# Optimization experiments

Hardware: AMD Instinct MI355X
Metric: run time of the kernel (lower is better)

## Reference

```python
import jax, jax.numpy as jnp
import numpy as np

B, MAXF, NFEAT, FT_OUT = 16384, 32, 768, 1024

def setup_inputs() -> dict:
    key = jax.random.key(0)
    k1, k2, k3, k4, k5, k6 = jax.random.split(key, 6)
    values = jnp.ones((B, MAXF), dtype=jnp.float32)
    stm_indices = jax.random.randint(k1, (B, MAXF), 0, NFEAT, dtype=jnp.int32)
    nstm_indices = jax.random.randint(k2, (B, MAXF), 0, NFEAT, dtype=jnp.int32)
    ft_w = jax.random.normal(k3, (NFEAT, FT_OUT), dtype=jnp.float32) * 0.02
    ft_b = jax.random.normal(k4, (FT_OUT,), dtype=jnp.float32) * 0.02
    out_w = jax.random.normal(k5, (2 * FT_OUT, 1), dtype=jnp.float32) * 0.02
    out_b = jax.random.normal(k6, (1,), dtype=jnp.float32) * 0.02
    return {"values": values, "stm_indices": stm_indices, "nstm_indices": nstm_indices,
            "ft_w": ft_w, "ft_b": ft_b, "out_w": out_w, "out_b": out_b}

def _ft_slice(indices, values, ft_w, ft_b):
    # sparse gather-accumulate: [B, MAXF] indices into [NFEAT, FT_OUT] table
    gathered = jnp.take(ft_w, indices, axis=0)          # [B, MAXF, FT_OUT]
    return jnp.einsum('bf,bfd->bd', values, gathered) + ft_b  # [B, FT_OUT]

def reference(values, stm_indices, nstm_indices, ft_w, ft_b, out_w, out_b):
    stm_ft = _ft_slice(stm_indices, values, ft_w, ft_b)
    nstm_ft = _ft_slice(nstm_indices, values, ft_w, ft_b)
    hidden = jnp.clip(jnp.concatenate([stm_ft, nstm_ft], axis=1), 0.0, 1.0)
    return jax.nn.sigmoid(hidden @ out_w + out_b)  # [B, 1]
```

## Files before the change

### kernel.cpp

```cpp
#include <hip/hip_runtime.h>
#include <hip/hip_fp16.h>
#include <math.h>

#define BATCH 16384
#define MAXF 32
#define NFEAT 768
#define FT_OUT 1024
#define CHUNK 32
#define NCHUNK (FT_OUT / CHUNK)
#define GROUPS 24
#define CH_ELEMS (NFEAT * CHUNK)

#define GET4(a, f) (((f) & 3) == 0 ? (a)[(f) >> 2].x : \
                    ((f) & 3) == 1 ? (a)[(f) >> 2].y : \
                    ((f) & 3) == 2 ? (a)[(f) >> 2].z : (a)[(f) >> 2].w)

__global__ __launch_bounds__(256) void convert_kernel(const float* __restrict__ ft_w,
                                                      __half* __restrict__ tab) {
    const int i = (blockIdx.x * 256 + threadIdx.x) * 4;
    const int r = i >> 10;
    const int col = i & 1023;
    const int c = col >> 5;
    const int within = col & 31;
    float4 f = *(const float4*)(ft_w + i);
    __half2 lo = __floats2half2_rn(f.x, f.y);
    __half2 hi = __floats2half2_rn(f.z, f.w);
    __half2* dst = (__half2*)(tab + (size_t)c * CH_ELEMS + r * CHUNK + within);
    dst[0] = lo;
    dst[1] = hi;
}

__global__ __launch_bounds__(256, 3) void nnboard_main(
    const float* __restrict__ values,
    const int*   __restrict__ stm_idx,
    const int*   __restrict__ nstm_idx,
    const __half* __restrict__ tab,
    const float* __restrict__ ft_b,
    const float* __restrict__ out_w,
    float*       __restrict__ logits)
{
    __shared__ __half s_tab[CH_ELEMS];

    const int tid = threadIdx.x;
    const int c = blockIdx.x % NCHUNK;
    const int g = blockIdx.x / NCHUNK;

    {
        const uint4* src = (const uint4*)(tab + (size_t)c * CH_ELEMS);
        uint4* dst = (uint4*)s_tab;
        #pragma unroll
        for (int k = 0; k < CH_ELEMS / 8 / 256; ++k)
            dst[k * 256 + tid] = src[k * 256 + tid];
    }
    __syncthreads();

    const int grp = tid >> 2;
    const int j   = tid & 3;
    const int col0 = c * CHUNK + j * 8;
    const __half* my_tab = s_tab + j * 8;

    const float4 bia0 = *(const float4*)(ft_b + col0);
    const float4 bia1 = *(const float4*)(ft_b + col0 + 4);
    const float4 ws0  = *(const float4*)(out_w + col0);
    const float4 ws1  = *(const float4*)(out_w + col0 + 4);
    const float4 wn0  = *(const float4*)(out_w + FT_OUT + col0);
    const float4 wn1  = *(const float4*)(out_w + FT_OUT + col0 + 4);

    const __half2 zero2 = __float2half2_rn(0.f);

    for (int it = g; it < BATCH / 64; it += GROUPS) {
        const int b = it * 64 + grp;

        const int4*   sp = (const int4*)(stm_idx + b * MAXF);
        const int4*   np = (const int4*)(nstm_idx + b * MAXF);
        const float4* vp = (const float4*)(values + b * MAXF);
        int4 si[8], ni[8];
        float4 vv[8];
        #pragma unroll
        for (int k = 0; k < 8; ++k) { si[k] = sp[k]; ni[k] = np[k]; vv[k] = vp[k]; }

        __half2 accs[4] = {zero2, zero2, zero2, zero2};
        __half2 accn[4] = {zero2, zero2, zero2, zero2};

        #pragma unroll
        for (int f = 0; f < MAXF; ++f) {
            const int is = GET4(si, f);
            const int in = GET4(ni, f);
            const __half2 v2 = __float2half2_rn(GET4(vv, f));
            const uint4 qs = *(const uint4*)(my_tab + is * CHUNK);
            const uint4 qn = *(const uint4*)(my_tab + in * CHUNK);
            accs[0] = __hfma2(*(const __half2*)&qs.x, v2, accs[0]);
            accs[1] = __hfma2(*(const __half2*)&qs.y, v2, accs[1]);
            accs[2] = __hfma2(*(const __half2*)&qs.z, v2, accs[2]);
            accs[3] = __hfma2(*(const __half2*)&qs.w, v2, accs[3]);
            accn[0] = __hfma2(*(const __half2*)&qn.x, v2, accn[0]);
            accn[1] = __hfma2(*(const __half2*)&qn.y, v2, accn[1]);
            accn[2] = __hfma2(*(const __half2*)&qn.z, v2, accn[2]);
            accn[3] = __hfma2(*(const __half2*)&qn.w, v2, accn[3]);
        }

        float p = 0.f;
        {
            const float2 f0 = __half22float2(accs[0]);
            const float2 f1 = __half22float2(accs[1]);
            const float2 f2 = __half22float2(accs[2]);
            const float2 f3 = __half22float2(accs[3]);
            const float2 g0 = __half22float2(accn[0]);
            const float2 g1 = __half22float2(accn[1]);
            const float2 g2 = __half22float2(accn[2]);
            const float2 g3 = __half22float2(accn[3]);
            auto clip = [](float x) { return fminf(fmaxf(x, 0.f), 1.f); };
            p = fmaf(clip(f0.x + bia0.x), ws0.x, p);
            p = fmaf(clip(f0.y + bia0.y), ws0.y, p);
            p = fmaf(clip(f1.x + bia0.z), ws0.z, p);
            p = fmaf(clip(f1.y + bia0.w), ws0.w, p);
            p = fmaf(clip(f2.x + bia1.x), ws1.x, p);
            p = fmaf(clip(f2.y + bia1.y), ws1.y, p);
            p = fmaf(clip(f3.x + bia1.z), ws1.z, p);
            p = fmaf(clip(f3.y + bia1.w), ws1.w, p);
            p = fmaf(clip(g0.x + bia0.x), wn0.x, p);
            p = fmaf(clip(g0.y + bia0.y), wn0.y, p);
            p = fmaf(clip(g1.x + bia0.z), wn0.z, p);
            p = fmaf(clip(g1.y + bia0.w), wn0.w, p);
            p = fmaf(clip(g2.x + bia1.x), wn1.x, p);
            p = fmaf(clip(g2.y + bia1.y), wn1.y, p);
            p = fmaf(clip(g3.x + bia1.z), wn1.z, p);
            p = fmaf(clip(g3.y + bia1.w), wn1.w, p);
        }

        p += __shfl_down(p, 1, 64);
        p += __shfl_down(p, 2, 64);
        if (j == 0) atomicAdd(logits + b, p);
    }
}

__global__ __launch_bounds__(256) void sigmoid_kernel(const float* __restrict__ logits,
                                                      const float* __restrict__ out_b,
                                                      float* __restrict__ out) {
    const int i = blockIdx.x * 256 + threadIdx.x;
    out[i] = 1.f / (1.f + expf(-(logits[i] + out_b[0])));
}

extern "C" void kernel_launch(void* const* d_in, const int* in_sizes, int n_in,
                              void* d_out, int out_size, void* d_ws, size_t ws_size,
                              hipStream_t stream) {
    const float* values   = (const float*)d_in[0];
    const int*   stm_idx  = (const int*)d_in[1];
    const int*   nstm_idx = (const int*)d_in[2];
    const float* ft_w     = (const float*)d_in[3];
    const float* ft_b     = (const float*)d_in[4];
    const float* out_w    = (const float*)d_in[5];
    const float* out_b    = (const float*)d_in[6];
    float*       out      = (float*)d_out;

    __half* tab    = (__half*)d_ws;
    float*  logits = (float*)((char*)d_ws + (size_t)NCHUNK * CH_ELEMS * 2);

    convert_kernel<<<(NFEAT * FT_OUT) / (256 * 4), 256, 0, stream>>>(ft_w, tab);
    hipMemsetAsync(logits, 0, BATCH * sizeof(float), stream);
    nnboard_main<<<NCHUNK * GROUPS, 256, 0, stream>>>(
        values, stm_idx, nstm_idx, tab, ft_b, out_w, logits);
    sigmoid_kernel<<<BATCH / 256, 256, 0, stream>>>(logits, out_b, out);
}
```

Before: 112.5 us.

## Fuse weight conversion and sigmoid into main kernel with padded LDS rows

Removes the separate fp32-to-fp16 conversion kernel and instead converts each chunk of ft_w directly while loading it into shared memory. Table rows are padded to 40 halves to reduce LDS bank conflicts on the random gathers. The sigmoid kernel is folded in through per-row arrival counters, so the last chunk block to finish a row applies out_b and the sigmoid. GROUPS drops from 24 to 16 and the occupancy hint from 3 to 2 blocks per CU to fit the larger LDS footprint. In exchange each block reads fp32 weights from global memory, and the kernel adds a threadfence plus extra counter atomics.

After: 157.6 us. 40.0% more time.

```diff
diff --git a/kernel.cpp b/kernel.cpp
--- a/kernel.cpp
+++ b/kernel.cpp
@@ -8,49 +8,48 @@
 #define FT_OUT 1024
 #define CHUNK 32
 #define NCHUNK (FT_OUT / CHUNK)
-#define GROUPS 24
-#define CH_ELEMS (NFEAT * CHUNK)
+#define GROUPS 16
+#define PAD 40
+#define CH_HALVES (NFEAT * PAD)
 
 #define GET4(a, f) (((f) & 3) == 0 ? (a)[(f) >> 2].x : \
                     ((f) & 3) == 1 ? (a)[(f) >> 2].y : \
                     ((f) & 3) == 2 ? (a)[(f) >> 2].z : (a)[(f) >> 2].w)
 
-__global__ __launch_bounds__(256) void convert_kernel(const float* __restrict__ ft_w,
-                                                      __half* __restrict__ tab) {
-    const int i = (blockIdx.x * 256 + threadIdx.x) * 4;
-    const int r = i >> 10;
-    const int col = i & 1023;
-    const int c = col >> 5;
-    const int within = col & 31;
-    float4 f = *(const float4*)(ft_w + i);
-    __half2 lo = __floats2half2_rn(f.x, f.y);
-    __half2 hi = __floats2half2_rn(f.z, f.w);
-    __half2* dst = (__half2*)(tab + (size_t)c * CH_ELEMS + r * CHUNK + within);
-    dst[0] = lo;
-    dst[1] = hi;
-}
+typedef unsigned int uint_t;
 
-__global__ __launch_bounds__(256, 3) void nnboard_main(
+__global__ __launch_bounds__(256, 2) void nnboard_main(
     const float* __restrict__ values,
     const int*   __restrict__ stm_idx,
     const int*   __restrict__ nstm_idx,
-    const __half* __restrict__ tab,
+    const float* __restrict__ ft_w,
     const float* __restrict__ ft_b,
     const float* __restrict__ out_w,
-    float*       __restrict__ logits)
+    const float* __restrict__ out_b,
+    float*       __restrict__ logits,
+    int*         __restrict__ counts,
+    float*       __restrict__ out)
 {
-    __shared__ __half s_tab[CH_ELEMS];
+    __shared__ __half s_tab[CH_HALVES];
 
     const int tid = threadIdx.x;
     const int c = blockIdx.x % NCHUNK;
     const int g = blockIdx.x / NCHUNK;
 
     {
-        const uint4* src = (const uint4*)(tab + (size_t)c * CH_ELEMS);
-        uint4* dst = (uint4*)s_tab;
+        const int lane8 = tid & 7;
+        const int rbase = tid >> 3;
         #pragma unroll
-        for (int k = 0; k < CH_ELEMS / 8 / 256; ++k)
-            dst[k * 256 + tid] = src[k * 256 + tid];
+        for (int k = 0; k < NFEAT / 32; ++k) {
+            const int r = k * 32 + rbase;
+            const float4 f = *(const float4*)(ft_w + (size_t)r * FT_OUT + c * CHUNK + lane8 * 4);
+            __half2 h0 = __floats2half2_rn(f.x, f.y);
+            __half2 h1 = __floats2half2_rn(f.z, f.w);
+            uint2 u;
+            u.x = *reinterpret_cast<uint_t*>(&h0);
+            u.y = *reinterpret_cast<uint_t*>(&h1);
+            *(uint2*)(s_tab + r * PAD + lane8 * 4) = u;
+        }
     }
     __syncthreads();
 
@@ -65,6 +64,7 @@
     const float4 ws1  = *(const float4*)(out_w + col0 + 4);
     const float4 wn0  = *(const float4*)(out_w + FT_OUT + col0);
     const float4 wn1  = *(const float4*)(out_w + FT_OUT + col0 + 4);
+    const float ob = out_b[0];
 
     const __half2 zero2 = __float2half2_rn(0.f);
 
@@ -87,8 +87,8 @@
             const int is = GET4(si, f);
             const int in = GET4(ni, f);
             const __half2 v2 = __float2half2_rn(GET4(vv, f));
-            const uint4 qs = *(const uint4*)(my_tab + is * CHUNK);
-            const uint4 qn = *(const uint4*)(my_tab + in * CHUNK);
+            const uint4 qs = *(const uint4*)(my_tab + is * PAD);
+            const uint4 qn = *(const uint4*)(my_tab + in * PAD);
             accs[0] = __hfma2(*(const __half2*)&qs.x, v2, accs[0]);
             accs[1] = __hfma2(*(const __half2*)&qs.y, v2, accs[1]);
             accs[2] = __hfma2(*(const __half2*)&qs.z, v2, accs[2]);
@@ -132,13 +132,20 @@
         p += __shfl_down(p, 2, 64);
         if (j == 0) atomicAdd(logits + b, p);
     }
-}
 
-__global__ __launch_bounds__(256) void sigmoid_kernel(const float* __restrict__ logits,
-                                                      const float* __restrict__ out_b,
-                                                      float* __restrict__ out) {
-    const int i = blockIdx.x * 256 + threadIdx.x;
-    out[i] = 1.f / (1.f + expf(-(logits[i] + out_b[0])));
+    __threadfence();
+    __syncthreads();
+
+    if (tid < 64) {
+        for (int it = g; it < BATCH / 64; it += GROUPS) {
+            const int b = it * 64 + tid;
+            const int cnt = atomicAdd(counts + b, 1);
+            if (cnt == NCHUNK - 1) {
+                const float l = atomicAdd(logits + b, 0.f);
+                out[b] = 1.f / (1.f + expf(-(l + ob)));
+            }
+        }
+    }
 }
 
 extern "C" void kernel_launch(void* const* d_in, const int* in_sizes, int n_in,
@@ -153,12 +160,10 @@
     const float* out_b    = (const float*)d_in[6];
     float*       out      = (float*)d_out;
 
-    __half* tab    = (__half*)d_ws;
-    float*  logits = (float*)((char*)d_ws + (size_t)NCHUNK * CH_ELEMS * 2);
+    float* logits = (float*)d_ws;
+    int*   counts = (int*)((char*)d_ws + BATCH * sizeof(float));
 
-    convert_kernel<<<(NFEAT * FT_OUT) / (256 * 4), 256, 0, stream>>>(ft_w, tab);
-    hipMemsetAsync(logits, 0, BATCH * sizeof(float), stream);
+    hipMemsetAsync(d_ws, 0, 2 * BATCH * sizeof(float), stream);
     nnboard_main<<<NCHUNK * GROUPS, 256, 0, stream>>>(
-        values, stm_idx, nstm_idx, tab, ft_b, out_w, logits);
-    sigmoid_kernel<<<BATCH / 256, 256, 0, stream>>>(logits, out_b, out);
+        values, stm_idx, nstm_idx, ft_w, ft_b, out_w, out_b, logits, counts, out);
 }
```
